# Performance work log

Hardware: AMD Instinct MI355X
Metric: run time of the kernel (lower is better)

## Reference

```python
import jax, jax.numpy as jnp
import numpy as np


def setup_inputs() -> dict:
    key = jax.random.key(0)
    k1, k2 = jax.random.split(key)
    B, D, H, W = 32, 64, 32, 32
    K = 1024
    z_e = jax.random.normal(k1, (B, D, H, W), dtype=jnp.float32)
    # original init: uniform(-1/K, 1/K); use same scale
    emb = jax.random.uniform(k2, (K, D), dtype=jnp.float32, minval=-1.0 / K, maxval=1.0 / K)
    return {"z_e": z_e, "emb": emb}


COMMITMENT_COST = 0.25


def reference(z_e, emb):
    # z_e: [B, D, H, W], emb: [K, D]
    B, D, H, W = z_e.shape
    K = emb.shape[0]
    z = jnp.transpose(z_e, (0, 2, 3, 1))           # [B, H, W, D]
    flat = z.reshape(-1, D)                        # [N, D]
    N = flat.shape[0]

    dist = (
        jnp.sum(flat * flat, axis=1, keepdims=True)
        + jnp.sum(emb * emb, axis=1)
        - 2.0 * flat @ emb.T
    )
    idx = jnp.argmin(dist, axis=1)                 # [N]
    encodings = jax.nn.one_hot(idx, K, dtype=flat.dtype)  # [N, K]
    z_q = (encodings @ emb).reshape(z.shape)       # [B, H, W, D]

    e_latent_loss = jnp.mean((jax.lax.stop_gradient(z_q) - z) ** 2)
    q_latent_loss = jnp.mean((z_q - jax.lax.stop_gradient(z)) ** 2)
    loss = q_latent_loss + COMMITMENT_COST * e_latent_loss

    # straight-through estimator
    z_st = z + jax.lax.stop_gradient(z_q - z)

    avg_probs = jnp.sum(encodings, axis=0) / jnp.float32(N)
    perplexity = jnp.exp(-jnp.sum(avg_probs * jnp.log(avg_probs + 1e-10)))

    return (jnp.transpose(z_st, (0, 3, 1, 2)), loss, perplexity, encodings)
```

## Files before the change

kernel.cpp:

```cpp
#include <hip/hip_runtime.h>
#include <stdint.h>
#include <math.h>

constexpr int Nn  = 32768;
constexpr int Kk  = 1024;

constexpr int OUT0_N   = 32 * 64 * 1024;
constexpr int OUT_LOSS = OUT0_N;
constexpr int OUT_PERP = OUT0_N + 1;
constexpr int OUT_ENC  = OUT0_N + 2;

constexpr size_t WS_CNT = 0;
constexpr size_t WS_LP  = 4096;
constexpr size_t WS_KEY = 69632;

__device__ __forceinline__ float norm64v(const float4* __restrict__ p) {
#pragma clang fp contract(off)
    float tt[64];
#pragma unroll
    for (int q = 0; q < 16; ++q) {
        float4 v = p[q];
        tt[4 * q + 0] = v.x * v.x;
        tt[4 * q + 1] = v.y * v.y;
        tt[4 * q + 2] = v.z * v.z;
        tt[4 * q + 3] = v.w * v.w;
    }
    float r[8];
#pragma unroll
    for (int j = 0; j < 8; ++j) r[j] = tt[j];
#pragma unroll
    for (int i = 8; i < 64; i += 8)
#pragma unroll
        for (int j = 0; j < 8; ++j) r[j] += tt[i + j];
    return ((r[0] + r[1]) + (r[2] + r[3])) + ((r[4] + r[5]) + (r[6] + r[7]));
}

__device__ __forceinline__ uint32_t fsort(float f) {
    uint32_t b = __float_as_uint(f);
    return (b & 0x80000000u) ? ~b : (b | 0x80000000u);
}

__global__ __launch_bounds__(256, 2)
void dist_kernel(const float* __restrict__ z_e, const float* __restrict__ emb,
                 unsigned long long* __restrict__ minkey,
                 uint32_t* __restrict__ counts,
                 float* __restrict__ out) {
    __shared__ float xs[128 * 68];
    __shared__ float es[128 * 68];
    __shared__ float An_s[128];
    __shared__ float Bn_s[128];
    const int tid = threadIdx.x;
    const int rg = blockIdx.x >> 3, cg = blockIdx.x & 7;
    const int n0 = rg * 128;
    const int b = n0 >> 10, hw0 = n0 & 1023;
    const float* zb = z_e + (size_t)b * 65536 + hw0;

    {
        int hwi = tid & 127;
        int d4g = tid >> 7;
#pragma unroll
        for (int it = 0; it < 8; ++it) {
            int dbase = (d4g + it * 2) * 4;
            float4 v;
            v.x = zb[(size_t)(dbase + 0) * 1024 + hwi];
            v.y = zb[(size_t)(dbase + 1) * 1024 + hwi];
            v.z = zb[(size_t)(dbase + 2) * 1024 + hwi];
            v.w = zb[(size_t)(dbase + 3) * 1024 + hwi];
            *(float4*)&xs[hwi * 68 + dbase] = v;
        }
    }
    {
        const float4* ep = (const float4*)(emb + (size_t)cg * 128 * 64);
#pragma unroll
        for (int it = 0; it < 8; ++it) {
            int j = tid + it * 256;
            float4 v = ep[j];
            int c = j >> 4, d4 = j & 15;
            *(float4*)&es[c * 68 + d4 * 4] = v;
        }
    }
    if (blockIdx.x == 0) {
        ((uint4*)counts)[tid] = make_uint4(0u, 0u, 0u, 0u);
    }
    __syncthreads();

    if (tid < 128) {
        An_s[tid] = norm64v((const float4*)&xs[tid * 68]);
    } else {
        int c = tid - 128;
        Bn_s[c] = norm64v((const float4*)&es[c * 68]);
    }
    __syncthreads();

    {
        float4 z4 = make_float4(0.0f, 0.0f, 0.0f, 0.0f);
        float4* encz = (float4*)(out + OUT_ENC) + (size_t)blockIdx.x * 4096;
#pragma unroll
        for (int it = 0; it < 16; ++it) encz[it * 256 + tid] = z4;
    }

    const int tx = tid & 15, ty = tid >> 4;
    float acc[8][8];
#pragma unroll
    for (int i = 0; i < 8; ++i)
#pragma unroll
        for (int j = 0; j < 8; ++j) acc[i][j] = 0.0f;

#pragma unroll 1
    for (int d4 = 0; d4 < 16; ++d4) {
        float4 xv[8], ev[8];
#pragma unroll
        for (int i = 0; i < 8; ++i) xv[i] = *(const float4*)&xs[(ty + 16 * i) * 68 + d4 * 4];
#pragma unroll
        for (int j = 0; j < 8; ++j) ev[j] = *(const float4*)&es[(tx + 16 * j) * 68 + d4 * 4];
#pragma unroll
        for (int i = 0; i < 8; ++i)
#pragma unroll
            for (int j = 0; j < 8; ++j) {
                float a = acc[i][j];
                a = __builtin_fmaf(xv[i].x, ev[j].x, a);
                a = __builtin_fmaf(xv[i].y, ev[j].y, a);
                a = __builtin_fmaf(xv[i].z, ev[j].z, a);
                a = __builtin_fmaf(xv[i].w, ev[j].w, a);
                acc[i][j] = a;
            }
    }

    float Ar[8], Bc[8];
#pragma unroll
    for (int i = 0; i < 8; ++i) Ar[i] = An_s[ty + 16 * i];
#pragma unroll
    for (int j = 0; j < 8; ++j) Bc[j] = Bn_s[tx + 16 * j];

#pragma unroll
    for (int i = 0; i < 8; ++i) {
        unsigned long long best = ~0ULL;
#pragma unroll
        for (int j = 0; j < 8; ++j) {
            float s = Ar[i] + Bc[j];
            float dist = s - 2.0f * acc[i][j];
            unsigned long long key = ((unsigned long long)fsort(dist) << 32)
                                   | (unsigned)(cg * 128 + tx + 16 * j);
            best = (key < best) ? key : best;
        }
#pragma unroll
        for (int m = 1; m < 16; m <<= 1) {
            unsigned long long o = __shfl_xor(best, m, 64);
            best = (o < best) ? o : best;
        }
        if (tx == 0) atomicMin(&minkey[n0 + ty + 16 * i], best);
    }
}

__global__ __launch_bounds__(256)
void finish_kernel(const float* __restrict__ z_e,
                   const float* __restrict__ emb,
                   const unsigned long long* __restrict__ minkey,
                   uint32_t* __restrict__ counts,
                   double* __restrict__ lp,
                   float* __restrict__ out) {
    __shared__ uint32_t scode[64];
    __shared__ double lred[4];
    const int t = threadIdx.x;
    const int n0 = blockIdx.x * 64;
    const int b = n0 >> 10, hw0 = n0 & 1023;

    if (t < 64) {
        uint32_t code = (uint32_t)minkey[n0 + t];
        scode[t] = code;
        atomicAdd(&counts[code], 1u);
        out[(size_t)OUT_ENC + (size_t)(n0 + t) * 1024 + code] = 1.0f;
    }
    __syncthreads();

    const int hwi = t & 63, dg = t >> 6;
    const uint32_t code = scode[hwi];
    const float4* er4 = (const float4*)(emb + (size_t)code * 64) + dg * 4;
    const size_t base = (size_t)b * 65536 + (size_t)(dg * 16) * 1024 + hw0 + hwi;

    double ls = 0.0;
#pragma unroll
    for (int k4 = 0; k4 < 4; ++k4) {
        float4 e4 = er4[k4];
        float f0 = e4.x, f1 = e4.y, f2 = e4.z, f3 = e4.w;
        size_t off = base + (size_t)(k4 * 4) * 1024;
        {
            float z = z_e[off];            float tt = f0 - z;
            out[off] = z + tt;             ls += (double)tt * (double)tt;
        }
        {
            float z = z_e[off + 1024];     float tt = f1 - z;
            out[off + 1024] = z + tt;      ls += (double)tt * (double)tt;
        }
        {
            float z = z_e[off + 2048];     float tt = f2 - z;
            out[off + 2048] = z + tt;      ls += (double)tt * (double)tt;
        }
        {
            float z = z_e[off + 3072];     float tt = f3 - z;
            out[off + 3072] = z + tt;      ls += (double)tt * (double)tt;
        }
    }
#pragma unroll
    for (int m = 32; m >= 1; m >>= 1) ls += __shfl_down(ls, m, 64);
    if ((t & 63) == 0) lred[t >> 6] = ls;
    __syncthreads();
    if (t == 0) lp[blockIdx.x] = lred[0] + lred[1] + lred[2] + lred[3];
}

__global__ void scalar_kernel(const uint32_t* __restrict__ counts,
                              const double* __restrict__ lp,
                              float* __restrict__ out) {
    __shared__ double redl[4], redh[4];
    const int t = threadIdx.x;
    double ls = 0.0;
    for (int i = t; i < 512; i += 256) ls += lp[i];
    double h = 0.0;
    for (int i = t; i < Kk; i += 256) {
        double p = (double)counts[i] * (1.0 / 32768.0);
        h += p * log(p + 1e-10);
    }
#pragma unroll
    for (int m = 32; m >= 1; m >>= 1) { ls += __shfl_down(ls, m, 64); h += __shfl_down(h, m, 64); }
    if ((t & 63) == 0) { redl[t >> 6] = ls; redh[t >> 6] = h; }
    __syncthreads();
    if (t == 0) {
        double L = redl[0] + redl[1] + redl[2] + redl[3];
        double H = redh[0] + redh[1] + redh[2] + redh[3];
        out[OUT_PERP] = (float)exp(-H);
        float m32 = (float)(L * (1.0 / 2097152.0));
        out[OUT_LOSS] = m32 + 0.25f * m32;
    }
}

extern "C" void kernel_launch(void* const* d_in, const int* in_sizes, int n_in,
                              void* d_out, int out_size, void* d_ws, size_t ws_size,
                              hipStream_t stream) {
    const float* z_e = (const float*)d_in[0];
    const float* emb = (const float*)d_in[1];
    float* out = (float*)d_out;
    char* ws = (char*)d_ws;

    uint32_t* counts = (uint32_t*)(ws + WS_CNT);
    double*   lp     = (double*)(ws + WS_LP);
    unsigned long long* minkey = (unsigned long long*)(ws + WS_KEY);

    hipMemsetAsync(ws + WS_KEY, 0xFF, (size_t)Nn * 8, stream);

    dist_kernel<<<2048, 256, 0, stream>>>(z_e, emb, minkey, counts, out);
    finish_kernel<<<512, 256, 0, stream>>>(z_e, emb, minkey, counts, lp, out);
    scalar_kernel<<<1, 256, 0, stream>>>(counts, lp, out);
}
```

Baseline: 214.7 us.

## Use bf16 MFMA distance screening with exact fp32 re-rank of near-tie candidates

```diff
diff --git a/kernel.cpp b/kernel.cpp
--- a/kernel.cpp
+++ b/kernel.cpp
@@ -2,7 +2,6 @@
 #include <stdint.h>
 #include <math.h>
 
-constexpr int Nn  = 32768;
 constexpr int Kk  = 1024;
 
 constexpr int OUT0_N   = 32 * 64 * 1024;
@@ -12,7 +11,11 @@
 
 constexpr size_t WS_CNT = 0;
 constexpr size_t WS_LP  = 4096;
-constexpr size_t WS_KEY = 69632;
+constexpr size_t WS_BN  = 8192;
+constexpr size_t WS_RI  = 12288;
+
+typedef short bf16x8 __attribute__((ext_vector_type(8)));
+typedef float f32x16 __attribute__((ext_vector_type(16)));
 
 __device__ __forceinline__ float norm64v(const float4* __restrict__ p) {
 #pragma clang fp contract(off)
@@ -40,170 +43,302 @@
     return (b & 0x80000000u) ? ~b : (b | 0x80000000u);
 }
 
-__global__ __launch_bounds__(256, 2)
-void dist_kernel(const float* __restrict__ z_e, const float* __restrict__ emb,
-                 unsigned long long* __restrict__ minkey,
-                 uint32_t* __restrict__ counts,
-                 float* __restrict__ out) {
-    __shared__ float xs[128 * 68];
-    __shared__ float es[128 * 68];
-    __shared__ float An_s[128];
-    __shared__ float Bn_s[128];
-    const int tid = threadIdx.x;
-    const int rg = blockIdx.x >> 3, cg = blockIdx.x & 7;
-    const int n0 = rg * 128;
-    const int b = n0 >> 10, hw0 = n0 & 1023;
-    const float* zb = z_e + (size_t)b * 65536 + hw0;
+__device__ __forceinline__ unsigned short f2bf(float f) {
+    uint32_t u = __float_as_uint(f);
+    uint32_t r = (u + 0x7fffu + ((u >> 16) & 1u)) >> 16;
+    return (unsigned short)r;
+}
+
+__global__ __launch_bounds__(256, 1)
+void dist_mfma(const float* __restrict__ z_e, const float* __restrict__ emb,
+               uint32_t* __restrict__ rowinfo, uint32_t* __restrict__ counts,
+               float* __restrict__ Bn_g, float* __restrict__ out) {
+    __shared__ unsigned short ebf[1024 * 64];
+    __shared__ float Bn_s[1024];
+    __shared__ float wmax[4];
+    const int t = threadIdx.x;
+    const int lane = t & 63, wv = t >> 6;
+    const int g = lane >> 5;
+    const int n0 = blockIdx.x * 128;
+    const int b = n0 >> 10;
+    const int hw = (n0 & 1023) + wv * 32 + (lane & 31);
 
     {
-        int hwi = tid & 127;
-        int d4g = tid >> 7;
-#pragma unroll
-        for (int it = 0; it < 8; ++it) {
-            int dbase = (d4g + it * 2) * 4;
-            float4 v;
-            v.x = zb[(size_t)(dbase + 0) * 1024 + hwi];
-            v.y = zb[(size_t)(dbase + 1) * 1024 + hwi];
-            v.z = zb[(size_t)(dbase + 2) * 1024 + hwi];
-            v.w = zb[(size_t)(dbase + 3) * 1024 + hwi];
-            *(float4*)&xs[hwi * 68 + dbase] = v;
-        }
-    }
-    {
-        const float4* ep = (const float4*)(emb + (size_t)cg * 128 * 64);
-#pragma unroll
-        for (int it = 0; it < 8; ++it) {
-            int j = tid + it * 256;
-            float4 v = ep[j];
-            int c = j >> 4, d4 = j & 15;
-            *(float4*)&es[c * 68 + d4 * 4] = v;
-        }
-    }
+        const float4* e4 = (const float4*)emb;
+#pragma unroll 8
+        for (int it = 0; it < 64; ++it) {
+            int j = t + it * 256;
+            float4 v = e4[j];
+            int code = j >> 4, q = j & 15;
+            ushort4 bv;
+            bv.x = f2bf(v.x); bv.y = f2bf(v.y); bv.z = f2bf(v.z); bv.w = f2bf(v.w);
+            int byte = code * 128 + ((q * 8) ^ ((code & 7) << 4));
+            *(ushort4*)((char*)ebf + byte) = bv;
+        }
+    }
+
+    float mymax = 0.f;
+#pragma unroll
+    for (int i = 0; i < 4; ++i) {
+        int code = t + i * 256;
+        float nn = norm64v((const float4*)(emb + (size_t)code * 64));
+        Bn_s[code] = nn;
+        mymax = fmaxf(mymax, nn);
+    }
+#pragma unroll
+    for (int m = 1; m < 64; m <<= 1) mymax = fmaxf(mymax, __shfl_xor(mymax, m, 64));
+    if (lane == 0) wmax[wv] = mymax;
     if (blockIdx.x == 0) {
-        ((uint4*)counts)[tid] = make_uint4(0u, 0u, 0u, 0u);
-    }
-    __syncthreads();
-
-    if (tid < 128) {
-        An_s[tid] = norm64v((const float4*)&xs[tid * 68]);
-    } else {
-        int c = tid - 128;
-        Bn_s[c] = norm64v((const float4*)&es[c * 68]);
-    }
-    __syncthreads();
-
-    {
-        float4 z4 = make_float4(0.0f, 0.0f, 0.0f, 0.0f);
-        float4* encz = (float4*)(out + OUT_ENC) + (size_t)blockIdx.x * 4096;
-#pragma unroll
-        for (int it = 0; it < 16; ++it) encz[it * 256 + tid] = z4;
-    }
-
-    const int tx = tid & 15, ty = tid >> 4;
-    float acc[8][8];
-#pragma unroll
-    for (int i = 0; i < 8; ++i)
-#pragma unroll
-        for (int j = 0; j < 8; ++j) acc[i][j] = 0.0f;
-
+        ((uint4*)counts)[t] = make_uint4(0u, 0u, 0u, 0u);
+    }
+    __syncthreads();
+    const float maxBn = fmaxf(fmaxf(wmax[0], wmax[1]), fmaxf(wmax[2], wmax[3]));
+    if (blockIdx.x == 0) {
+#pragma unroll
+        for (int i = 0; i < 4; ++i) Bn_g[t + i * 256] = Bn_s[t + i * 256];
+    }
+
+    bf16x8 bfrag[4];
+    float xsq = 0.f;
+    const float* zb = z_e + (size_t)b * 65536 + hw;
+#pragma unroll
+    for (int s = 0; s < 4; ++s) {
+        bf16x8 f;
+#pragma unroll
+        for (int e = 0; e < 8; ++e) {
+            int d = s * 16 + g * 8 + e;
+            float x = zb[(size_t)d * 1024];
+            xsq = __builtin_fmaf(x, x, xsq);
+            f[e] = (short)f2bf(x);
+        }
+        bfrag[s] = f;
+    }
+    xsq += __shfl_xor(xsq, 32, 64);
+    const float margin = 0.017f * sqrtf(xsq * maxBn) + 1.0e-4f;
+
+    const int swz = (lane & 7) << 4;
+    const int offs[4] = { (0 * 32 + g * 16) ^ swz, (1 * 32 + g * 16) ^ swz,
+                          (2 * 32 + g * 16) ^ swz, (3 * 32 + g * 16) ^ swz };
+    const char* ebase = (const char*)ebf + (lane & 31) * 128;
+
+    auto tile_acc = [&](int c) -> f32x16 {
+        const char* p = ebase + c * 4096;
+        bf16x8 a0 = *(const bf16x8*)(p + offs[0]);
+        bf16x8 a1 = *(const bf16x8*)(p + offs[1]);
+        bf16x8 a2 = *(const bf16x8*)(p + offs[2]);
+        bf16x8 a3 = *(const bf16x8*)(p + offs[3]);
+        f32x16 acc = {};
+        acc = __builtin_amdgcn_mfma_f32_32x32x16_bf16(a0, bfrag[0], acc, 0, 0, 0);
+        acc = __builtin_amdgcn_mfma_f32_32x32x16_bf16(a1, bfrag[1], acc, 0, 0, 0);
+        acc = __builtin_amdgcn_mfma_f32_32x32x16_bf16(a2, bfrag[2], acc, 0, 0, 0);
+        acc = __builtin_amdgcn_mfma_f32_32x32x16_bf16(a3, bfrag[3], acc, 0, 0, 0);
+        return acc;
+    };
+
+    float4* encz = (float4*)(out + OUT_ENC) + (size_t)blockIdx.x * 32768;
+    const float4 zero4 = make_float4(0.f, 0.f, 0.f, 0.f);
+
+    float runmin = 3.4e38f;
 #pragma unroll 1
-    for (int d4 = 0; d4 < 16; ++d4) {
-        float4 xv[8], ev[8];
-#pragma unroll
-        for (int i = 0; i < 8; ++i) xv[i] = *(const float4*)&xs[(ty + 16 * i) * 68 + d4 * 4];
-#pragma unroll
-        for (int j = 0; j < 8; ++j) ev[j] = *(const float4*)&es[(tx + 16 * j) * 68 + d4 * 4];
-#pragma unroll
-        for (int i = 0; i < 8; ++i)
-#pragma unroll
-            for (int j = 0; j < 8; ++j) {
-                float a = acc[i][j];
-                a = __builtin_fmaf(xv[i].x, ev[j].x, a);
-                a = __builtin_fmaf(xv[i].y, ev[j].y, a);
-                a = __builtin_fmaf(xv[i].z, ev[j].z, a);
-                a = __builtin_fmaf(xv[i].w, ev[j].w, a);
-                acc[i][j] = a;
-            }
-    }
-
-    float Ar[8], Bc[8];
-#pragma unroll
-    for (int i = 0; i < 8; ++i) Ar[i] = An_s[ty + 16 * i];
-#pragma unroll
-    for (int j = 0; j < 8; ++j) Bc[j] = Bn_s[tx + 16 * j];
-
-#pragma unroll
-    for (int i = 0; i < 8; ++i) {
-        unsigned long long best = ~0ULL;
-#pragma unroll
-        for (int j = 0; j < 8; ++j) {
-            float s = Ar[i] + Bc[j];
-            float dist = s - 2.0f * acc[i][j];
-            unsigned long long key = ((unsigned long long)fsort(dist) << 32)
-                                   | (unsigned)(cg * 128 + tx + 16 * j);
-            best = (key < best) ? key : best;
-        }
-#pragma unroll
-        for (int m = 1; m < 16; m <<= 1) {
-            unsigned long long o = __shfl_xor(best, m, 64);
-            best = (o < best) ? o : best;
-        }
-        if (tx == 0) atomicMin(&minkey[n0 + ty + 16 * i], best);
+    for (int c = 0; c < 32; ++c) {
+        f32x16 acc = tile_acc(c);
+        encz[(size_t)(c * 2 + 0) * 256 + t] = zero4;
+        encz[(size_t)(c * 2 + 1) * 256 + t] = zero4;
+        float tm = 3.4e38f;
+#pragma unroll
+        for (int r = 0; r < 16; ++r) {
+            int code = c * 32 + (r & 3) + 8 * (r >> 2) + 4 * g;
+            float sv = __builtin_fmaf(-2.f, acc[r], Bn_s[code]);
+            tm = fminf(tm, sv);
+        }
+        runmin = fminf(runmin, tm);
+    }
+    runmin = fminf(runmin, __shfl_xor(runmin, 32, 64));
+    const float thr = runmin + margin;
+
+    uint32_t cnt = 0, cc0 = 0, cc1 = 0, cc2 = 0;
+#pragma unroll 1
+    for (int c = 0; c < 32; ++c) {
+        f32x16 acc = tile_acc(c);
+        encz[(size_t)(64 + c * 2 + 0) * 256 + t] = zero4;
+        encz[(size_t)(64 + c * 2 + 1) * 256 + t] = zero4;
+#pragma unroll
+        for (int r = 0; r < 16; ++r) {
+            int code = c * 32 + (r & 3) + 8 * (r >> 2) + 4 * g;
+            float sv = __builtin_fmaf(-2.f, acc[r], Bn_s[code]);
+            if (sv <= thr) {
+                if (cnt == 0) cc0 = (uint32_t)code;
+                else if (cnt == 1) cc1 = (uint32_t)code;
+                else if (cnt == 2) cc2 = (uint32_t)code;
+                ++cnt;
+            }
+        }
+    }
+    uint32_t pcnt = __shfl_xor(cnt, 32, 64);
+    uint32_t p0 = __shfl_xor(cc0, 32, 64);
+    uint32_t p1 = __shfl_xor(cc1, 32, 64);
+    uint32_t p2 = __shfl_xor(cc2, 32, 64);
+    if (lane < 32) {
+        uint32_t tot = cnt + pcnt;
+        uint32_t info;
+        if (cnt > 3u || pcnt > 3u || tot > 3u) {
+            info = 3u << 30;
+        } else {
+            uint32_t ownm = (cnt >= 3u) ? 0x3FFFFFFFu : ((1u << (cnt * 10)) - 1u);
+            uint32_t prtm = (pcnt >= 3u) ? 0x3FFFFFFFu : ((1u << (pcnt * 10)) - 1u);
+            uint32_t ownp = (cc0 | (cc1 << 10) | (cc2 << 20)) & ownm;
+            uint32_t prtp = (p0 | (p1 << 10) | (p2 << 20)) & prtm;
+            info = ((tot - 1u) << 30) | ownp | (prtp << (cnt * 10));
+        }
+        rowinfo[n0 + wv * 32 + lane] = info;
     }
 }
 
 __global__ __launch_bounds__(256)
-void finish_kernel(const float* __restrict__ z_e,
-                   const float* __restrict__ emb,
-                   const unsigned long long* __restrict__ minkey,
-                   uint32_t* __restrict__ counts,
-                   double* __restrict__ lp,
+void finish_kernel(const float* __restrict__ z_e, const float* __restrict__ emb,
+                   const uint32_t* __restrict__ rowinfo,
+                   const float* __restrict__ Bn_g,
+                   uint32_t* __restrict__ counts, double* __restrict__ lp,
                    float* __restrict__ out) {
+    __shared__ float zs[64 * 68];
     __shared__ uint32_t scode[64];
+    __shared__ unsigned long long pkey[64][3];
+    __shared__ uint32_t pairbuf[192];
+    __shared__ unsigned long long rbuf[4];
     __shared__ double lred[4];
+    __shared__ uint32_t npairs, novf, ovfrow[8];
     const int t = threadIdx.x;
     const int n0 = blockIdx.x * 64;
     const int b = n0 >> 10, hw0 = n0 & 1023;
+    if (t == 0) { npairs = 0u; novf = 0u; }
+    const int hwi = t & 63, dg = t >> 6;
+
+    float zreg[16];
+    const size_t base = (size_t)b * 65536 + (size_t)(dg * 16) * 1024 + hw0 + hwi;
+#pragma unroll
+    for (int k = 0; k < 16; ++k) zreg[k] = z_e[base + (size_t)k * 1024];
+#pragma unroll
+    for (int m = 0; m < 4; ++m) {
+        float4 v = make_float4(zreg[4 * m], zreg[4 * m + 1], zreg[4 * m + 2], zreg[4 * m + 3]);
+        *(float4*)&zs[hwi * 68 + dg * 16 + 4 * m] = v;
+    }
+    __syncthreads();
 
     if (t < 64) {
-        uint32_t code = (uint32_t)minkey[n0 + t];
-        scode[t] = code;
+        uint32_t info = rowinfo[n0 + t];
+        uint32_t c = (info >> 30) + 1u;
+        if (c == 1u) {
+            scode[t] = info & 1023u;
+        } else if (c <= 3u) {
+            uint32_t bs = atomicAdd(&npairs, c);
+#pragma unroll
+            for (uint32_t i = 0; i < 3; ++i)
+                if (i < c)
+                    pairbuf[bs + i] = ((uint32_t)t << 16) | (i << 12) | ((info >> (10u * i)) & 1023u);
+        } else {
+            uint32_t o = atomicAdd(&novf, 1u);
+            if (o < 8u) ovfrow[o] = (uint32_t)t;
+        }
+    }
+    __syncthreads();
+
+    if (t < (int)npairs) {
+        uint32_t p = pairbuf[t];
+        int row = (int)(p >> 16), slot = (int)((p >> 12) & 3u), code = (int)(p & 1023u);
+        const float* xr = &zs[row * 68];
+        const float* er = emb + (size_t)code * 64;
+        float c = 0.f;
+#pragma unroll
+        for (int d = 0; d < 64; ++d) c = __builtin_fmaf(xr[d], er[d], c);
+        float A = norm64v((const float4*)xr);
+        float s = A + Bn_g[code];
+        float dist = __builtin_fmaf(-2.f, c, s);
+        pkey[row][slot] = ((unsigned long long)fsort(dist) << 32) | (unsigned)code;
+    }
+    __syncthreads();
+
+    {
+        uint32_t no = novf < 8u ? novf : 8u;
+        for (uint32_t o = 0; o < no; ++o) {
+            int row = (int)ovfrow[o];
+            const float* xr = &zs[row * 68];
+            float A = norm64v((const float4*)xr);
+            unsigned long long best = ~0ULL;
+#pragma unroll 1
+            for (int cc = 0; cc < 4; ++cc) {
+                int code = t + cc * 256;
+                const float* er = emb + (size_t)code * 64;
+                float c = 0.f;
+#pragma unroll
+                for (int d = 0; d < 64; ++d) c = __builtin_fmaf(xr[d], er[d], c);
+                float s = A + Bn_g[code];
+                float dist = __builtin_fmaf(-2.f, c, s);
+                unsigned long long key = ((unsigned long long)fsort(dist) << 32) | (unsigned)code;
+                best = (key < best) ? key : best;
+            }
+#pragma unroll
+            for (int m = 1; m < 64; m <<= 1) {
+                unsigned long long ok = __shfl_xor(best, m, 64);
+                best = (ok < best) ? ok : best;
+            }
+            if ((t & 63) == 0) rbuf[t >> 6] = best;
+            __syncthreads();
+            if (t == 0) {
+                unsigned long long bb = rbuf[0];
+#pragma unroll
+                for (int w = 1; w < 4; ++w) bb = (rbuf[w] < bb) ? rbuf[w] : bb;
+                scode[row] = (uint32_t)bb;
+            }
+            __syncthreads();
+        }
+    }
+    if (t < 64) {
+        uint32_t info = rowinfo[n0 + t];
+        uint32_t c = (info >> 30) + 1u;
+        if (c >= 2u && c <= 3u) {
+            unsigned long long bb = pkey[t][0];
+            if (c > 1u && pkey[t][1] < bb) bb = pkey[t][1];
+            if (c > 2u && pkey[t][2] < bb) bb = pkey[t][2];
+            scode[t] = (uint32_t)bb;
+        }
+    }
+    __syncthreads();
+
+    if (t < 64) {
+        uint32_t code = scode[t];
         atomicAdd(&counts[code], 1u);
         out[(size_t)OUT_ENC + (size_t)(n0 + t) * 1024 + code] = 1.0f;
     }
-    __syncthreads();
-
-    const int hwi = t & 63, dg = t >> 6;
-    const uint32_t code = scode[hwi];
-    const float4* er4 = (const float4*)(emb + (size_t)code * 64) + dg * 4;
-    const size_t base = (size_t)b * 65536 + (size_t)(dg * 16) * 1024 + hw0 + hwi;
-
-    double ls = 0.0;
-#pragma unroll
-    for (int k4 = 0; k4 < 4; ++k4) {
-        float4 e4 = er4[k4];
-        float f0 = e4.x, f1 = e4.y, f2 = e4.z, f3 = e4.w;
-        size_t off = base + (size_t)(k4 * 4) * 1024;
-        {
-            float z = z_e[off];            float tt = f0 - z;
-            out[off] = z + tt;             ls += (double)tt * (double)tt;
-        }
-        {
-            float z = z_e[off + 1024];     float tt = f1 - z;
-            out[off + 1024] = z + tt;      ls += (double)tt * (double)tt;
-        }
-        {
-            float z = z_e[off + 2048];     float tt = f2 - z;
-            out[off + 2048] = z + tt;      ls += (double)tt * (double)tt;
-        }
-        {
-            float z = z_e[off + 3072];     float tt = f3 - z;
-            out[off + 3072] = z + tt;      ls += (double)tt * (double)tt;
-        }
-    }
-#pragma unroll
-    for (int m = 32; m >= 1; m >>= 1) ls += __shfl_down(ls, m, 64);
-    if ((t & 63) == 0) lred[t >> 6] = ls;
+
+    {
+        const uint32_t code = scode[hwi];
+        const float4* er4 = (const float4*)(emb + (size_t)code * 64) + dg * 4;
+        double ls = 0.0;
+#pragma unroll
+        for (int k4 = 0; k4 < 4; ++k4) {
+            float4 e4 = er4[k4];
+            float fe0 = e4.x, fe1 = e4.y, fe2 = e4.z, fe3 = e4.w;
+            {
+                float z = zreg[k4 * 4 + 0]; float tt = fe0 - z;
+                out[base + (size_t)(k4 * 4 + 0) * 1024] = z + tt; ls += (double)tt * (double)tt;
+            }
+            {
+                float z = zreg[k4 * 4 + 1]; float tt = fe1 - z;
+                out[base + (size_t)(k4 * 4 + 1) * 1024] = z + tt; ls += (double)tt * (double)tt;
+            }
+            {
+                float z = zreg[k4 * 4 + 2]; float tt = fe2 - z;
+                out[base + (size_t)(k4 * 4 + 2) * 1024] = z + tt; ls += (double)tt * (double)tt;
+            }
+            {
+                float z = zreg[k4 * 4 + 3]; float tt = fe3 - z;
+                out[base + (size_t)(k4 * 4 + 3) * 1024] = z + tt; ls += (double)tt * (double)tt;
+            }
+        }
+#pragma unroll
+        for (int m = 32; m >= 1; m >>= 1) ls += __shfl_down(ls, m, 64);
+        if ((t & 63) == 0) lred[t >> 6] = ls;
+    }
     __syncthreads();
     if (t == 0) lp[blockIdx.x] = lred[0] + lred[1] + lred[2] + lred[3];
 }
@@ -241,13 +376,12 @@
     float* out = (float*)d_out;
     char* ws = (char*)d_ws;
 
-    uint32_t* counts = (uint32_t*)(ws + WS_CNT);
-    double*   lp     = (double*)(ws + WS_LP);
-    unsigned long long* minkey = (unsigned long long*)(ws + WS_KEY);
-
-    hipMemsetAsync(ws + WS_KEY, 0xFF, (size_t)Nn * 8, stream);
-
-    dist_kernel<<<2048, 256, 0, stream>>>(z_e, emb, minkey, counts, out);
-    finish_kernel<<<512, 256, 0, stream>>>(z_e, emb, minkey, counts, lp, out);
+    uint32_t* counts  = (uint32_t*)(ws + WS_CNT);
+    double*   lp      = (double*)(ws + WS_LP);
+    float*    Bn_g    = (float*)(ws + WS_BN);
+    uint32_t* rowinfo = (uint32_t*)(ws + WS_RI);
+
+    dist_mfma<<<256, 256, 0, stream>>>(z_e, emb, rowinfo, counts, Bn_g, out);
+    finish_kernel<<<512, 256, 0, stream>>>(z_e, emb, rowinfo, Bn_g, counts, lp, out);
     scalar_kernel<<<1, 256, 0, stream>>>(counts, lp, out);
 }
```

Result: slower. 254.8 us (+18.7%).
